# Kernel tuning notes

Measured on AMD Instinct MI355X. Metric: run time of the kernel, lower is better.

The kernel has to match this reference:

```python
import jax, jax.numpy as jnp
import numpy as np

B, D, H, C, T = 65536, 512, 256, 100, 10
EPS = 0.01  # halt_epsilon


def setup_inputs() -> dict:
    key = jax.random.key(0)
    ks = jax.random.split(key, 10)
    sD = 1.0 / np.sqrt(D)
    sH = 1.0 / np.sqrt(H)
    return {
        "x": jax.random.normal(ks[0], (B, D), dtype=jnp.float32),
        # GRUCell params (PyTorch layout: rows chunked as [r; z; n])
        "W_ih": jax.random.uniform(ks[1], (3 * H, D), minval=-sD, maxval=sD, dtype=jnp.float32),
        "W_hh": jax.random.uniform(ks[2], (3 * H, H), minval=-sH, maxval=sH, dtype=jnp.float32),
        "b_ih": jax.random.uniform(ks[3], (3 * H,), minval=-sH, maxval=sH, dtype=jnp.float32),
        "b_hh": jax.random.uniform(ks[4], (3 * H,), minval=-sH, maxval=sH, dtype=jnp.float32),
        # halting unit
        "W_halt": jax.random.uniform(ks[5], (1, H), minval=-sH, maxval=sH, dtype=jnp.float32),
        "b_halt": jax.random.uniform(ks[6], (1,), minval=-sH, maxval=sH, dtype=jnp.float32),
        # readout
        "W_ro": jax.random.uniform(ks[7], (C, H), minval=-sH, maxval=sH, dtype=jnp.float32),
        "b_ro": jax.random.uniform(ks[8], (C,), minval=-sH, maxval=sH, dtype=jnp.float32),
    }


def _act_forward(x, W_ih, W_hh, b_ih, b_hh, W_halt, b_halt, W_ro, b_ro):
    dt = x.dtype
    thresh = jnp.asarray(1.0 - EPS, dt)
    # x is static across ponder steps -> precompute input projection once
    x_proj = x @ W_ih.T + b_ih                       # [B, 3H]
    xr, xz, xn = jnp.split(x_proj, 3, axis=-1)

    def step(carry, _):
        h, cum, rem, nup, acc = carry
        h_proj = h @ W_hh.T + b_hh                   # [B, 3H]
        hr, hz, hn = jnp.split(h_proj, 3, axis=-1)
        r = jax.nn.sigmoid(xr + hr)
        z = jax.nn.sigmoid(xz + hz)
        n = jnp.tanh(xn + r * hn)
        h_new = (1.0 - z) * n + z * h                # GRUCell update
        halt = jax.nn.sigmoid(h_new @ W_halt.T + b_halt)[:, 0]  # [B]
        logits_t = h_new @ W_ro.T + b_ro             # [B, C]
        still = (cum < thresh).astype(dt)
        new_halt = halt * still
        would = (cum + new_halt > thresh).astype(dt)
        remainder = (1.0 - cum) * would * still
        step_w = new_halt * (1.0 - would) + remainder
        cum2 = cum + step_w
        acc2 = acc + step_w[:, None] * h_new
        return (h_new, cum2, rem + remainder, nup + still, acc2), (h_new, halt, logits_t)

    zB = jnp.zeros((x.shape[0],), dt)
    init = (jnp.zeros((x.shape[0], W_hh.shape[1]), dt), zB, zB, zB,
            jnp.zeros((x.shape[0], W_hh.shape[1]), dt))
    (h, cum, remainders, n_updates, acc), (h_seq, halt_seq, logits_seq) = jax.lax.scan(
        step, init, None, length=T)
    logits = acc @ W_ro.T + b_ro                     # [B, C]
    ponder_cost = n_updates.mean() + remainders.mean()
    # scan stacks on axis 0 (time) -> move to dim 1 as torch.stack(dim=1)
    h_seq = jnp.swapaxes(h_seq, 0, 1)                # [B, T, H]
    halt_seq = jnp.swapaxes(halt_seq, 0, 1)          # [B, T]
    logits_seq = jnp.swapaxes(logits_seq, 0, 1)      # [B, T, C]
    return logits, ponder_cost, n_updates, h_seq, halt_seq, logits_seq


def reference(x, W_ih, W_hh, b_ih, b_hh, W_halt, b_halt, W_ro, b_ro):
    return _act_forward(x, W_ih, W_hh, b_ih, b_hh, W_halt, b_halt, W_ro, b_ro)
```

## Files before the change

### kernel.cpp

```cpp
#include <hip/hip_runtime.h>
#include <cmath>


namespace {
constexpr int B = 65536, D = 512, H = 256, C = 100, T = 10;

constexpr long OUT_LOGITS = 0;
constexpr long OUT_PONDER = (long)B * C;
constexpr long OUT_NUP    = OUT_PONDER + 1;
constexpr long OUT_HSEQ   = OUT_NUP + B;
constexpr long OUT_HALT   = OUT_HSEQ + (long)B * T * H;
constexpr long OUT_LSEQ   = OUT_HALT + (long)B * T;

constexpr long NIH  = 768L * D;
constexpr long NHH  = 768L * H;
constexpr long NAUG = 112L * H;

constexpr long WS_XP   = 0;
constexpr long WS_W16  = WS_XP + (long)B * 768;
constexpr long W_HALV  = 2 * (NIH + NHH + NAUG);
constexpr long WS_HL   = WS_W16 + (W_HALV + 1) / 2;
constexpr long WS_HP4  = WS_HL + (long)B * T;
constexpr long WS_NUPB = WS_HP4 + 4L * B * T;
constexpr long WS_REMB = WS_NUPB + B;
constexpr long WS_H16  = WS_REMB + B;
constexpr long H16_PER_T = 512L * 65536;

constexpr float SC = 256.f;
constexpr float SB = 1.f / 65536.f;
}

typedef __attribute__((ext_vector_type(8))) _Float16 h8;
typedef __attribute__((ext_vector_type(4))) _Float16 h4;
typedef __attribute__((ext_vector_type(4))) float f4;

#define MFMA16(A, Bo, Cc) __builtin_amdgcn_mfma_f32_16x16x32_f16(A, Bo, Cc, 0, 0, 0)
#define PROD3(a, Ah, Al, Bh, Bl)                                               \
  a = MFMA16(Al, Bh, a);                                                       \
  a = MFMA16(Ah, Bl, a);                                                       \
  a = MFMA16(Ah, Bh, a);

__device__ __forceinline__ float sigmoidf_(float x) {
  if (x >= 0.f) { return 1.f / (1.f + expf(-x)); }
  float e = expf(x);
  return e / (1.f + e);
}

__device__ __forceinline__ void gload_lds16(const _Float16* g, _Float16* l) {
  __builtin_amdgcn_global_load_lds(
      (const __attribute__((address_space(1))) unsigned int*)g,
      (__attribute__((address_space(3))) unsigned int*)l, 16, 0, 0);
}

__global__ void k_prep(const float* __restrict__ wih_s, const float* __restrict__ whh_s,
                       const float* __restrict__ wro, const float* __restrict__ whalt,
                       _Float16* __restrict__ wr) {
  long idx = (long)blockIdx.x * 256 + threadIdx.x;
  if (idx < NIH) {
    float xs = wih_s[idx] * SC;
    _Float16 h = (_Float16)xs;
    _Float16 l = (_Float16)(xs - (float)h);
    wr[idx] = h; wr[NIH + idx] = l;
  }
  if (idx < NHH) {
    float xs = whh_s[idx] * SC;
    _Float16 h = (_Float16)xs;
    _Float16 l = (_Float16)(xs - (float)h);
    long b = 2 * NIH;
    wr[b + idx] = h; wr[b + NHH + idx] = l;
  }
  if (idx < NAUG) {
    int row = (int)(idx >> 8), k = (int)(idx & 255);
    float x = (row < C) ? wro[row * 256 + k] : ((row == C) ? whalt[k] : 0.f);
    float xs = x * SC;
    _Float16 h = (_Float16)xs;
    _Float16 l = (_Float16)(xs - (float)h);
    long b = 2 * (NIH + NHH);
    wr[b + idx] = h; wr[b + NAUG + idx] = l;
  }
}

__device__ __forceinline__ void stageA16(const float* __restrict__ src,
                                         _Float16* As0, _Float16* As1,
                                         int o) {
#pragma unroll
  for (int i = 0; i < 4; ++i) {
    float4 v = ((const float4*)src)[i];
    float vv[4] = {v.x, v.y, v.z, v.w};
    h4 hh, ll;
#pragma unroll
    for (int c = 0; c < 4; ++c) {
      float sv = vv[c] * SC;
      _Float16 h = (_Float16)sv;
      hh[c] = h;
      ll[c] = (_Float16)(sv - (float)h);
    }
    *(h4*)&As0[o + i * 4] = hh;
    *(h4*)&As1[o + i * 4] = ll;
  }
}

__global__ __launch_bounds__(256, 3) void k_xproj(
    const float* __restrict__ x, const _Float16* __restrict__ wih,
    const float* __restrict__ b_ih, float* __restrict__ xp) {
  __shared__ __align__(16) _Float16 As0[128 * 40], As1[128 * 40];
  __shared__ __align__(16) _Float16 Bs[2][192 * 32];
  const int tid = threadIdx.x;
  const int w = tid >> 6, l = tid & 63;
  const int lr = l & 15, lq = l >> 4;
  const int bid = blockIdx.x;
  const int gid = (bid & 7) * 256 + (bid >> 3);
  const int c0 = (gid & 3) * 64;
  const int rb = (gid >> 2) * 128;

  f4 acc[8][3];
#pragma unroll
  for (int i = 0; i < 8; ++i)
#pragma unroll
    for (int g = 0; g < 3; ++g) acc[i][g] = (f4)0.f;

  for (int kc = 0; kc < 16; ++kc) {
    const int k0 = kc * 32;
    __syncthreads();
    {
      const int row = tid >> 1, kk0 = (tid & 1) * 16;
      stageA16(x + (long)(rb + row) * D + k0 + kk0, As0, As1, row * 40 + kk0);
    }
#pragma unroll
    for (int j = 0; j < 6; ++j) {
      int chunk = w * 6 + j;
      int plane = chunk / 12;
      int rem = chunk - plane * 12;
      int scol = rem * 16 + (l >> 2);
      int kq = l & 3;
      int gcol = (scol >> 6) * 256 + c0 + (scol & 63);
      gload_lds16(wih + (long)plane * NIH + (long)gcol * D + k0 + kq * 8,
                  &Bs[plane][rem * 512]);
    }
    __syncthreads();
    h8 Bh[3], Bl[3];
#pragma unroll
    for (int g = 0; g < 3; ++g) {
      Bh[g] = *(const h8*)&Bs[0][(g * 64 + w * 16 + lr) * 32 + lq * 8];
      Bl[g] = *(const h8*)&Bs[1][(g * 64 + w * 16 + lr) * 32 + lq * 8];
    }
#pragma unroll
    for (int i = 0; i < 8; ++i) {
      h8 Ah = *(const h8*)&As0[(i * 16 + lr) * 40 + lq * 8];
      h8 Al = *(const h8*)&As1[(i * 16 + lr) * 40 + lq * 8];
#pragma unroll
      for (int g = 0; g < 3; ++g) { PROD3(acc[i][g], Ah, Al, Bh[g], Bl[g]); }
    }
  }
  const int ch = c0 + w * 16 + lr;
  float bi[3] = {b_ih[ch], b_ih[256 + ch], b_ih[512 + ch]};
#pragma unroll
  for (int i = 0; i < 8; ++i)
#pragma unroll
    for (int g = 0; g < 3; ++g)
#pragma unroll
      for (int reg = 0; reg < 4; ++reg) {
        long row = rb + i * 16 + lq * 4 + reg;
        xp[row * 768 + g * 256 + ch] = fmaf(acc[i][g][reg], SB, bi[g]);
      }
}

__global__ __launch_bounds__(256, 3) void k_gru(
    const _Float16* __restrict__ whh, const float* __restrict__ xp,
    const float* __restrict__ b_hh, const float* __restrict__ w_halt,
    float* __restrict__ out, _Float16* __restrict__ h16,
    float* __restrict__ hp4, int t) {
  __shared__ __align__(16) _Float16 As[2][128 * 32];
  __shared__ __align__(16) _Float16 Bs[2][192 * 32];
  __shared__ float lds_hp[128][4];
  const int tid = threadIdx.x;
  const int w = tid >> 6, l = tid & 63;
  const int lr = l & 15, lq = l >> 4;
  const int bid = blockIdx.x;
  const int gid = (bid & 7) * 256 + (bid >> 3);
  const int strip = gid & 3;
  const int c0 = strip * 64;
  const int rb = (gid >> 2) * 128;
  const long tilebase = (long)(rb >> 7) * 65536;

  f4 acc[8][3];
#pragma unroll
  for (int i = 0; i < 8; ++i)
#pragma unroll
    for (int g = 0; g < 3; ++g) acc[i][g] = (f4)0.f;

  if (t > 0) {
    const _Float16* h16r = h16 + (long)(t - 1) * H16_PER_T + tilebase;
    for (int kc = 0; kc < 8; ++kc) {
      const int k0 = kc * 32;
      __syncthreads();
#pragma unroll
      for (int j = 0; j < 4; ++j) {
        int c8 = w * 4 + j;
        int plane = c8 >> 3;
        int c = c8 & 7;
        gload_lds16(h16r + (long)kc * 8192 + plane * 4096 + c * 512 + l * 8,
                    &As[plane][c * 512]);
      }
#pragma unroll
      for (int j = 0; j < 6; ++j) {
        int chunk = w * 6 + j;
        int plane = chunk / 12;
        int rem = chunk - plane * 12;
        int scol = rem * 16 + (l >> 2);
        int kq = l & 3;
        int gcol = (scol >> 6) * 256 + c0 + (scol & 63);
        gload_lds16(whh + (long)plane * NHH + (long)gcol * H + k0 + kq * 8,
                    &Bs[plane][rem * 512]);
      }
      __syncthreads();
      h8 Bh[3], Bl[3];
#pragma unroll
      for (int g = 0; g < 3; ++g) {
        Bh[g] = *(const h8*)&Bs[0][(g * 64 + w * 16 + lr) * 32 + lq * 8];
        Bl[g] = *(const h8*)&Bs[1][(g * 64 + w * 16 + lr) * 32 + lq * 8];
      }
#pragma unroll
      for (int i = 0; i < 8; ++i) {
        h8 Ah = *(const h8*)&As[0][(i * 16 + lr) * 32 + lq * 8];
        h8 Al = *(const h8*)&As[1][(i * 16 + lr) * 32 + lq * 8];
#pragma unroll
        for (int g = 0; g < 3; ++g) { PROD3(acc[i][g], Ah, Al, Bh[g], Bl[g]); }
      }
    }
  }

  const int ch = c0 + w * 16 + lr;
  const float bhr = b_hh[ch], bhz = b_hh[256 + ch], bhn = b_hh[512 + ch];
  const float whv = w_halt[ch];
  const long h16c = (long)t * H16_PER_T + tilebase + (long)(ch >> 5) * 8192 + (ch & 31);
#pragma unroll
  for (int i = 0; i < 8; ++i)
#pragma unroll
    for (int reg = 0; reg < 4; ++reg) {
      const int rloc = i * 16 + lq * 4 + reg;
      const long row = rb + rloc;
      float xr = xp[row * 768 + ch];
      float xz = xp[row * 768 + 256 + ch];
      float xn = xp[row * 768 + 512 + ch];
      float ho = (t > 0) ? out[OUT_HSEQ + row * (T * H) + (long)(t - 1) * H + ch] : 0.f;
      float rr = sigmoidf_(xr + fmaf(acc[i][0][reg], SB, bhr));
      float zz = sigmoidf_(xz + fmaf(acc[i][1][reg], SB, bhz));
      float nn = tanhf(xn + rr * fmaf(acc[i][2][reg], SB, bhn));
      float hv = (1.f - zz) * nn + zz * ho;
      out[OUT_HSEQ + row * (T * H) + (long)t * H + ch] = hv;
      float sv = hv * SC;
      _Float16 hi = (_Float16)sv;
      _Float16 lo = (_Float16)(sv - (float)hi);
      h16[h16c + (long)rloc * 32] = hi;
      h16[h16c + 4096 + (long)rloc * 32] = lo;
      float p = hv * whv;
#pragma unroll
      for (int m = 1; m < 16; m <<= 1) p += __shfl_xor(p, m, 64);
      if (lr == 0) lds_hp[rloc][w] = p;
    }
  __syncthreads();
  if (tid < 128)
    hp4[((long)t * 4 + strip) * B + rb + tid] =
        ((lds_hp[tid][0] + lds_hp[tid][1]) + (lds_hp[tid][2] + lds_hp[tid][3]));
}

__global__ __launch_bounds__(256, 4) void k_lseq(
    const _Float16* __restrict__ h16, const _Float16* __restrict__ waug,
    const float* __restrict__ b_ro, float* __restrict__ lseq) {
  __shared__ __align__(16) _Float16 As[128 * 32];
  __shared__ __align__(16) _Float16 Bs[112 * 32];
  const int tid = threadIdx.x;
  const int w = tid >> 6, l = tid & 63;
  const int lr = l & 15, lq = l >> 4;
  const int t = blockIdx.x >> 9;
  const int btile = blockIdx.x & 511;
  const _Float16* h16r = h16 + (long)t * H16_PER_T + (long)btile * 65536;

  f4 acc[2][7];
#pragma unroll
  for (int i = 0; i < 2; ++i)
#pragma unroll
    for (int j = 0; j < 7; ++j) acc[i][j] = (f4)0.f;

  for (int kc = 0; kc < 8; ++kc) {
    const int k0 = kc * 32;
    __syncthreads();
#pragma unroll
    for (int j = 0; j < 2; ++j) {
      int c = w * 2 + j;
      gload_lds16(h16r + (long)kc * 8192 + c * 512 + l * 8, &As[c * 512]);
    }
#pragma unroll
    for (int j = 0; j < 2; ++j) {
      int chunk = w + j * 4;
      if (chunk < 7) {
        int scol = chunk * 16 + (l >> 2);
        int kq = l & 3;
        gload_lds16(waug + (long)scol * H + k0 + kq * 8, &Bs[chunk * 512]);
      }
    }
    __syncthreads();
    h8 Af[2];
#pragma unroll
    for (int i = 0; i < 2; ++i)
      Af[i] = *(const h8*)&As[(w * 32 + i * 16 + lr) * 32 + lq * 8];
#pragma unroll
    for (int j = 0; j < 7; ++j) {
      h8 Bf = *(const h8*)&Bs[(j * 16 + lr) * 32 + lq * 8];
#pragma unroll
      for (int i = 0; i < 2; ++i) acc[i][j] = MFMA16(Af[i], Bf, acc[i][j]);
    }
  }
#pragma unroll
  for (int j = 0; j < 7; ++j) {
    const int col = j * 16 + lr;
    if (col < C) {
      const float br = b_ro[col];
#pragma unroll
      for (int i = 0; i < 2; ++i)
#pragma unroll
        for (int reg = 0; reg < 4; ++reg) {
          long b = (long)btile * 128 + w * 32 + i * 16 + lq * 4 + reg;
          lseq[(b * T + t) * C + col] = fmaf(acc[i][j][reg], SB, br);
        }
    }
  }
}

__global__ void k_act(const float* __restrict__ hp4, const float* __restrict__ b_halt,
                      float* __restrict__ out, float* __restrict__ swb,
                      float* __restrict__ nupb, float* __restrict__ remb) {
  const long b = (long)blockIdx.x * 256 + threadIdx.x;
  const float bh = b_halt[0];
  float cum = 0.f, rem = 0.f, nu = 0.f;
#pragma unroll
  for (int t = 0; t < T; ++t) {
    float v = bh + hp4[((long)t * 4 + 0) * B + b] + hp4[((long)t * 4 + 1) * B + b] +
              hp4[((long)t * 4 + 2) * B + b] + hp4[((long)t * 4 + 3) * B + b];
    float halt = sigmoidf_(v);
    out[OUT_HALT + b * T + t] = halt;
    float still = (cum < 0.99f) ? 1.f : 0.f;
    float nh = halt * still;
    float would = ((cum + nh) > 0.99f) ? 1.f : 0.f;
    float rema = (1.f - cum) * would * still;
    float swv = nh * (1.f - would) + rema;
    cum += swv; rem += rema; nu += still;
    swb[b * T + t] = swv;
  }
  nupb[b] = nu; remb[b] = rem;
}

__global__ void k_logits(const float* __restrict__ lseq, const float* __restrict__ swb,
                         const float* __restrict__ b_ro, const float* __restrict__ nupb,
                         float* __restrict__ out) {
  const long b = blockIdx.x;
  const int tid = threadIdx.x;
  if (tid < C) {
    float br = b_ro[tid];
    float s = br;
#pragma unroll
    for (int t = 0; t < T; ++t) {
      float sw = swb[b * T + t];
      s = fmaf(sw, lseq[(b * T + t) * C + tid] - br, s);
    }
    out[OUT_LOGITS + b * C + tid] = s;
  } else if (tid == C) {
    out[OUT_NUP + b] = nupb[b];
  }
}

__global__ void k_ponder(const float* __restrict__ nupb, const float* __restrict__ remb,
                         float* __restrict__ out) {
  __shared__ float sm[4];
  float s = 0.f;
  for (int i = threadIdx.x; i < B; i += 256) s += nupb[i] + remb[i];
#pragma unroll
  for (int m = 1; m < 64; m <<= 1) s += __shfl_xor(s, m, 64);
  int w = threadIdx.x >> 6;
  if ((threadIdx.x & 63) == 0) sm[w] = s;
  __syncthreads();
  if (threadIdx.x == 0)
    out[OUT_PONDER] = (sm[0] + sm[1] + sm[2] + sm[3]) * (1.f / (float)B);
}

extern "C" void kernel_launch(void* const* d_in, const int* in_sizes, int n_in,
                              void* d_out, int out_size, void* d_ws, size_t ws_size,
                              hipStream_t stream) {
  const float* x      = (const float*)d_in[0];
  const float* W_ih   = (const float*)d_in[1];
  const float* W_hh   = (const float*)d_in[2];
  const float* b_ih   = (const float*)d_in[3];
  const float* b_hh   = (const float*)d_in[4];
  const float* W_halt = (const float*)d_in[5];
  const float* b_halt = (const float*)d_in[6];
  const float* W_ro   = (const float*)d_in[7];
  const float* b_ro   = (const float*)d_in[8];
  float* out = (float*)d_out;
  float* ws  = (float*)d_ws;

  float* xp        = ws + WS_XP;
  _Float16* w16    = (_Float16*)(ws + WS_W16);
  _Float16* wih16  = w16;
  _Float16* whh16  = w16 + 2 * NIH;
  _Float16* waug16 = w16 + 2 * (NIH + NHH);
  float* swb  = ws + WS_HL;
  float* hp4  = ws + WS_HP4;
  float* nupb = ws + WS_NUPB;
  float* remb = ws + WS_REMB;
  _Float16* h16 = (_Float16*)(ws + WS_H16);

  k_prep<<<(int)((NIH + 255) / 256), 256, 0, stream>>>(W_ih, W_hh, W_ro, W_halt, w16);
  k_xproj<<<2048, 256, 0, stream>>>(x, wih16, b_ih, xp);
  for (int t = 0; t < T; ++t)
    k_gru<<<2048, 256, 0, stream>>>(whh16, xp, b_hh, W_halt, out, h16, hp4, t);
  k_lseq<<<512 * T, 256, 0, stream>>>(h16, waug16, b_ro, out + OUT_LSEQ);
  k_act<<<B / 256, 256, 0, stream>>>(hp4, b_halt, out, swb, nupb, remb);
  k_logits<<<B, 128, 0, stream>>>(out + OUT_LSEQ, swb, b_ro, nupb, out);
  k_ponder<<<1, 256, 0, stream>>>(nupb, remb, out);
}
```

Measured before the change: 2.239 ms.

## Halve GRU row tile, seed accumulators with x-projection, read previous h from LDS

Shrinks the k_gru row tile from 128 to 64 rows and doubles the grid, which lowers accumulator register use so the launch bound can rise to 4 blocks per CU. The x-projection r/z terms are preloaded into the MFMA accumulators, pre-scaled to cancel the later SB factor. The previous hidden state is rebuilt from the split-fp16 tile already staged in LDS instead of being reread from the fp32 h_seq output. The h16 workspace layout changes to 64-row tiles, and k_lseq indexing is updated to match. The cost is that each block reloads the W_hh slices for half as many rows, and the previous h now comes from the fp16 hi/lo pair, which may differ slightly in precision from the fp32 value.

```diff
diff --git a/kernel.cpp b/kernel.cpp
--- a/kernel.cpp
+++ b/kernel.cpp
@@ -24,10 +24,11 @@
 constexpr long WS_NUPB = WS_HP4 + 4L * B * T;
 constexpr long WS_REMB = WS_NUPB + B;
 constexpr long WS_H16  = WS_REMB + B;
-constexpr long H16_PER_T = 512L * 65536;
-
-constexpr float SC = 256.f;
-constexpr float SB = 1.f / 65536.f;
+constexpr long H16_PER_T = 1024L * 32768;
+
+constexpr float SC  = 256.f;
+constexpr float ISC = 1.f / 256.f;
+constexpr float SB  = 1.f / 65536.f;
 }
 
 typedef __attribute__((ext_vector_type(8))) _Float16 h8;
@@ -165,29 +166,39 @@
       }
 }
 
-__global__ __launch_bounds__(256, 3) void k_gru(
+__global__ __launch_bounds__(256, 4) void k_gru(
     const _Float16* __restrict__ whh, const float* __restrict__ xp,
     const float* __restrict__ b_hh, const float* __restrict__ w_halt,
     float* __restrict__ out, _Float16* __restrict__ h16,
     float* __restrict__ hp4, int t) {
-  __shared__ __align__(16) _Float16 As[2][128 * 32];
+  __shared__ __align__(16) _Float16 As[2][64 * 32];
   __shared__ __align__(16) _Float16 Bs[2][192 * 32];
-  __shared__ float lds_hp[128][4];
+  __shared__ float lds_hp[64][4];
   const int tid = threadIdx.x;
   const int w = tid >> 6, l = tid & 63;
   const int lr = l & 15, lq = l >> 4;
   const int bid = blockIdx.x;
-  const int gid = (bid & 7) * 256 + (bid >> 3);
+  const int gid = (bid & 7) * 512 + (bid >> 3);
   const int strip = gid & 3;
   const int c0 = strip * 64;
-  const int rb = (gid >> 2) * 128;
-  const long tilebase = (long)(rb >> 7) * 65536;
-
-  f4 acc[8][3];
-#pragma unroll
-  for (int i = 0; i < 8; ++i)
-#pragma unroll
-    for (int g = 0; g < 3; ++g) acc[i][g] = (f4)0.f;
+  const int rb = (gid >> 2) * 64;
+  const long tilebase = (long)(rb >> 6) * 32768;
+  const int ch = c0 + w * 16 + lr;
+  const int kc_h = ch >> 5;
+
+  f4 acc[4][3];
+  float ho[4][4];
+#pragma unroll
+  for (int i = 0; i < 4; ++i) {
+#pragma unroll
+    for (int reg = 0; reg < 4; ++reg) {
+      long row = rb + i * 16 + lq * 4 + reg;
+      acc[i][0][reg] = xp[row * 768 + ch] * 65536.f;
+      acc[i][1][reg] = xp[row * 768 + 256 + ch] * 65536.f;
+      ho[i][reg] = 0.f;
+    }
+    acc[i][2] = (f4)0.f;
+  }
 
   if (t > 0) {
     const _Float16* h16r = h16 + (long)(t - 1) * H16_PER_T + tilebase;
@@ -195,12 +206,12 @@
       const int k0 = kc * 32;
       __syncthreads();
 #pragma unroll
-      for (int j = 0; j < 4; ++j) {
-        int c8 = w * 4 + j;
-        int plane = c8 >> 3;
-        int c = c8 & 7;
-        gload_lds16(h16r + (long)kc * 8192 + plane * 4096 + c * 512 + l * 8,
-                    &As[plane][c * 512]);
+      for (int j = 0; j < 2; ++j) {
+        int c = w * 2 + j;
+        int plane = c >> 2;
+        int cc = c & 3;
+        gload_lds16(h16r + (long)kc * 4096 + plane * 2048 + cc * 512 + l * 8,
+                    &As[plane][cc * 512]);
       }
 #pragma unroll
       for (int j = 0; j < 6; ++j) {
@@ -221,46 +232,52 @@
         Bl[g] = *(const h8*)&Bs[1][(g * 64 + w * 16 + lr) * 32 + lq * 8];
       }
 #pragma unroll
-      for (int i = 0; i < 8; ++i) {
+      for (int i = 0; i < 4; ++i) {
         h8 Ah = *(const h8*)&As[0][(i * 16 + lr) * 32 + lq * 8];
         h8 Al = *(const h8*)&As[1][(i * 16 + lr) * 32 + lq * 8];
 #pragma unroll
         for (int g = 0; g < 3; ++g) { PROD3(acc[i][g], Ah, Al, Bh[g], Bl[g]); }
       }
-    }
-  }
-
-  const int ch = c0 + w * 16 + lr;
+      if (kc == kc_h) {
+#pragma unroll
+        for (int i = 0; i < 4; ++i)
+#pragma unroll
+          for (int reg = 0; reg < 4; ++reg) {
+            int rloc = i * 16 + lq * 4 + reg;
+            ho[i][reg] = ((float)As[0][rloc * 32 + (ch & 31)] +
+                          (float)As[1][rloc * 32 + (ch & 31)]) * ISC;
+          }
+      }
+    }
+  }
+
   const float bhr = b_hh[ch], bhz = b_hh[256 + ch], bhn = b_hh[512 + ch];
   const float whv = w_halt[ch];
-  const long h16c = (long)t * H16_PER_T + tilebase + (long)(ch >> 5) * 8192 + (ch & 31);
-#pragma unroll
-  for (int i = 0; i < 8; ++i)
+  const long h16base = (long)t * H16_PER_T + tilebase + (long)kc_h * 4096 + (ch & 31);
+#pragma unroll
+  for (int i = 0; i < 4; ++i)
 #pragma unroll
     for (int reg = 0; reg < 4; ++reg) {
       const int rloc = i * 16 + lq * 4 + reg;
       const long row = rb + rloc;
-      float xr = xp[row * 768 + ch];
-      float xz = xp[row * 768 + 256 + ch];
       float xn = xp[row * 768 + 512 + ch];
-      float ho = (t > 0) ? out[OUT_HSEQ + row * (T * H) + (long)(t - 1) * H + ch] : 0.f;
-      float rr = sigmoidf_(xr + fmaf(acc[i][0][reg], SB, bhr));
-      float zz = sigmoidf_(xz + fmaf(acc[i][1][reg], SB, bhz));
+      float rr = sigmoidf_(fmaf(acc[i][0][reg], SB, bhr));
+      float zz = sigmoidf_(fmaf(acc[i][1][reg], SB, bhz));
       float nn = tanhf(xn + rr * fmaf(acc[i][2][reg], SB, bhn));
-      float hv = (1.f - zz) * nn + zz * ho;
+      float hv = (1.f - zz) * nn + zz * ho[i][reg];
       out[OUT_HSEQ + row * (T * H) + (long)t * H + ch] = hv;
       float sv = hv * SC;
       _Float16 hi = (_Float16)sv;
       _Float16 lo = (_Float16)(sv - (float)hi);
-      h16[h16c + (long)rloc * 32] = hi;
-      h16[h16c + 4096 + (long)rloc * 32] = lo;
+      h16[h16base + (long)rloc * 32] = hi;
+      h16[h16base + 2048 + (long)rloc * 32] = lo;
       float p = hv * whv;
 #pragma unroll
       for (int m = 1; m < 16; m <<= 1) p += __shfl_xor(p, m, 64);
       if (lr == 0) lds_hp[rloc][w] = p;
     }
   __syncthreads();
-  if (tid < 128)
+  if (tid < 64)
     hp4[((long)t * 4 + strip) * B + rb + tid] =
         ((lds_hp[tid][0] + lds_hp[tid][1]) + (lds_hp[tid][2] + lds_hp[tid][3]));
 }
@@ -289,7 +306,8 @@
 #pragma unroll
     for (int j = 0; j < 2; ++j) {
       int c = w * 2 + j;
-      gload_lds16(h16r + (long)kc * 8192 + c * 512 + l * 8, &As[c * 512]);
+      gload_lds16(h16r + (long)(c >> 2) * 32768 + (long)kc * 4096 + (c & 3) * 512 + l * 8,
+                  &As[c * 512]);
     }
 #pragma unroll
     for (int j = 0; j < 2; ++j) {
@@ -413,7 +431,7 @@
   k_prep<<<(int)((NIH + 255) / 256), 256, 0, stream>>>(W_ih, W_hh, W_ro, W_halt, w16);
   k_xproj<<<2048, 256, 0, stream>>>(x, wih16, b_ih, xp);
   for (int t = 0; t < T; ++t)
-    k_gru<<<2048, 256, 0, stream>>>(whh16, xp, b_hh, W_halt, out, h16, hp4, t);
+    k_gru<<<4096, 256, 0, stream>>>(whh16, xp, b_hh, W_halt, out, h16, hp4, t);
   k_lseq<<<512 * T, 256, 0, stream>>>(h16, waug16, b_ro, out + OUT_LSEQ);
   k_act<<<B / 256, 256, 0, stream>>>(hp4, b_halt, out, swb, nupb, remb);
   k_logits<<<B, 128, 0, stream>>>(out + OUT_LSEQ, swb, b_ro, nupb, out);
```

Result: faster. 2.192 ms (-2.1%).
